# Performance work log

Measured on AMD Instinct MI355X. Metric: run time of the kernel, lower is better.

## Reference

```python
import jax, jax.numpy as jnp
from jax import lax
import numpy as np

B, L_IN, L_OUT, N, COV = 16, 96, 24, 320, 4
E, H = 64, 128
CIN = E + COV


def setup_inputs() -> dict:
    key = jax.random.key(0)
    ks = jax.random.split(key, 16)
    s = 0.05
    inp = {
        'history_data': jax.random.normal(ks[0], (B, L_IN, N, 1 + COV), jnp.float32),
        'future_data': jax.random.normal(ks[1], (B, L_OUT, N, 1 + COV), jnp.float32),
        'We': jax.random.normal(ks[2], (E, 1), jnp.float32) * s,
        'be': jnp.zeros((E,), jnp.float32),
        'Wih0': jax.random.normal(ks[3], (4 * H, CIN), jnp.float32) * s,
        'Whh0': jax.random.normal(ks[4], (4 * H, H), jnp.float32) * s,
        'bih0': jnp.zeros((4 * H,), jnp.float32),
        'bhh0': jnp.zeros((4 * H,), jnp.float32),
        'Wih1': jax.random.normal(ks[5], (4 * H, H), jnp.float32) * s,
        'Whh1': jax.random.normal(ks[6], (4 * H, H), jnp.float32) * s,
        'bih1': jnp.zeros((4 * H,), jnp.float32),
        'bhh1': jnp.zeros((4 * H,), jnp.float32),
        'Wh': jax.random.normal(ks[7], (2, H), jnp.float32) * s,
        'bh': jnp.zeros((2,), jnp.float32),
        'train': 1,
    }
    return inp


def _run_layer(xs, Wih, Whh, bih, bhh):
    # xs: [T, BN, Cin] -> ys: [T, BN, H]
    h0 = jnp.zeros((xs.shape[1], Whh.shape[1]), xs.dtype)

    def step(carry, x):
        h, c = carry
        g = x @ Wih.T + bih + h @ Whh.T + bhh  # [BN, 4H]
        i, f, gg, o = jnp.split(g, 4, axis=-1)  # torch gate order i,f,g,o
        c = jax.nn.sigmoid(f) * c + jax.nn.sigmoid(i) * jnp.tanh(gg)
        h = jax.nn.sigmoid(o) * jnp.tanh(c)
        return (h, c), h

    (_, _), ys = lax.scan(step, (h0, h0), xs)
    return ys


def reference(history_data, future_data, We, be, Wih0, Whh0, bih0, bhh0,
              Wih1, Whh1, bih1, bhh1, Wh, bh, train):
    # train branch (teacher forcing): history_next is always ground truth
    T = L_IN + L_OUT
    tgt = jnp.concatenate([history_data[..., 0:1], future_data[..., 0:1]], axis=1)  # [B,T,N,1]
    cov = jnp.concatenate([history_data[..., 1:], future_data[..., 1:]], axis=1)   # [B,T,N,COV]
    # step t uses target at t-1 and covariates at t, for t = 1..T-1
    embed = tgt[:, :T - 1] @ We.T + be                       # [B,T-1,N,E]
    enc_in = jnp.concatenate([embed, cov[:, 1:T]], axis=-1)  # [B,T-1,N,CIN]
    xs = enc_in.transpose(1, 0, 2, 3).reshape(T - 1, B * N, CIN)
    ys = _run_layer(xs, Wih0, Whh0, bih0, bhh0)
    ys = _run_layer(ys, Wih1, Whh1, bih1, bhh1)
    hid = jax.nn.relu(ys)                                    # [T-1, BN, H]
    head = hid @ Wh.T + bh                                   # [T-1, BN, 2]
    mu = head[..., 0:1]
    sigma = jax.nn.softplus(head[..., 1:2])
    p = jnp.concatenate([mu, sigma], axis=-1)
    p = p[-L_OUT:].reshape(L_OUT, B, N, 2).transpose(1, 0, 2, 3)  # [B,L_out,N,2]
    return p
```

## Files before the change

### kernel.cpp

```cpp
#include <hip/hip_runtime.h>

typedef __bf16 bf16x8 __attribute__((ext_vector_type(8)));
typedef unsigned short us8 __attribute__((ext_vector_type(8)));
typedef float f32x4 __attribute__((ext_vector_type(4)));

#define NROW 32
#define A_STR 136
#define NSTEP 119

__device__ __forceinline__ unsigned short f2bf(float f){
  unsigned int x = __builtin_bit_cast(unsigned int, f);
  x += 0x7fffu + ((x >> 16) & 1u);
  return (unsigned short)(x >> 16);
}
__device__ __forceinline__ float bf2f(unsigned short s){
  unsigned int x = ((unsigned int)s) << 16;
  return __builtin_bit_cast(float, x);
}
__device__ __forceinline__ float sigm(float x){ return 1.0f/(1.0f + __expf(-x)); }
__device__ __forceinline__ float tanh_(float x){ float e = __expf(2.0f*x); return 1.0f - 2.0f/(e + 1.0f); }

__device__ __forceinline__ f32x4 MFMA(us8 a, us8 b, f32x4 c){
  return __builtin_amdgcn_mfma_f32_16x16x32_bf16(
      __builtin_bit_cast(bf16x8, a), __builtin_bit_cast(bf16x8, b), c, 0, 0, 0);
}

struct SharedMem {
  unsigned short A0[2][NROW*A_STR];
  unsigned short A1[2][NROW*A_STR];
  unsigned short Ax[2][NROW][32];
  unsigned short xw[512*8];
  float c_lds[2][2][512][4];
  float b1[512];
  float Wh2f[256];
  float red[NROW][16][2];
  float we_s[64];
  float be_s[64];
  float bh_s[2];
};

__global__ __launch_bounds__(512)
__attribute__((amdgpu_waves_per_eu(2, 2)))
void deepar_kernel(
    const float* __restrict__ hist, const float* __restrict__ fut,
    const float* __restrict__ We,   const float* __restrict__ be,
    const float* __restrict__ Wih0, const float* __restrict__ Whh0,
    const float* __restrict__ bih0, const float* __restrict__ bhh0,
    const float* __restrict__ Wih1, const float* __restrict__ Whh1,
    const float* __restrict__ bih1, const float* __restrict__ bhh1,
    const float* __restrict__ Wh,   const float* __restrict__ bh,
    float* __restrict__ out)
{
  __shared__ SharedMem S;
  const int tid = threadIdx.x;
  const int wg  = blockIdx.x;
  const int b   = wg / 10;
  const int n0  = (wg % 10) * NROW;
  const int w   = tid >> 6;
  const int l   = tid & 63;
  const int gq  = l >> 4;
  const int r   = l & 15;

  {
    us8 z = {0,0,0,0,0,0,0,0};
    us8* pA0 = (us8*)&S.A0[0][0];
    us8* pA1 = (us8*)&S.A1[0][0];
    for (int i = tid; i < 2*NROW*A_STR/8; i += 512){ pA0[i] = z; pA1[i] = z; }
    us8* pAx = (us8*)&S.Ax[0][0][0];
    for (int i = tid; i < 2*NROW*32/8; i += 512) pAx[i] = z;
    f32x4 zf = {0.f,0.f,0.f,0.f};
    #pragma unroll
    for (int q = 0; q < 4; ++q) *(f32x4*)&S.c_lds[q >> 1][q & 1][tid][0] = zf;
  }
  if (tid < 64)       S.we_s[tid]       = We[tid];
  else if (tid < 128) S.be_s[tid - 64]  = be[tid - 64];
  else if (tid < 384) S.Wh2f[tid - 128] = Wh[tid - 128];
  else if (tid < 386) S.bh_s[tid - 384] = bh[tid - 384];
  __syncthreads();

  {
    const float* wr = Wih0 + tid * 68;
    float u = 0.f, v = 0.f;
    #pragma unroll 8
    for (int e = 0; e < 64; ++e){
      float wv = wr[e];
      u = fmaf(wv, S.we_s[e], u);
      v = fmaf(wv, S.be_s[e], v);
    }
    v += bih0[tid] + bhh0[tid];
    unsigned short* xp = &S.xw[tid * 8];
    xp[0] = f2bf(u);
    xp[1] = f2bf(wr[64]); xp[2] = f2bf(wr[65]); xp[3] = f2bf(wr[66]); xp[4] = f2bf(wr[67]);
    xp[5] = f2bf(v);
    xp[6] = 0; xp[7] = 0;
    S.b1[tid] = bih1[tid] + bhh1[tid];
  }
  if (tid < 64){ int row = tid >> 1, bsel = tid & 1; S.Ax[bsel][row][5] = 0x3F80; }
  if (tid < 160){
    int srow, sch, tau;
    if (tid < 32){ srow = tid; sch = 0; tau = 0; }
    else { int k = tid - 32; srow = k >> 2; sch = 1 + (k & 3); tau = 1; }
    const float* p = hist + ((b*96 + tau)*320 + n0 + srow)*5;
    S.Ax[0][srow][sch] = f2bf(p[sch]);
  }

  us8 WB[3][4][4];
  #pragma unroll
  for (int m = 0; m < 3; ++m){
    const float* base = (m == 0) ? Whh0 : (m == 1) ? Wih1 : Whh1;
    #pragma unroll
    for (int g = 0; g < 4; ++g){
      int col = g*128 + w*16 + r;
      #pragma unroll
      for (int q = 0; q < 4; ++q){
        const float* p = base + col*128 + q*32 + gq*8;
        f32x4 x0 = *(const f32x4*)p;
        f32x4 x1 = *(const f32x4*)(p + 4);
        us8 tt;
        tt[0]=f2bf(x0[0]); tt[1]=f2bf(x0[1]); tt[2]=f2bf(x0[2]); tt[3]=f2bf(x0[3]);
        tt[4]=f2bf(x1[0]); tt[5]=f2bf(x1[1]); tt[6]=f2bf(x1[2]); tt[7]=f2bf(x1[3]);
        WB[m][g][q] = tt;
      }
    }
  }

  __syncthreads();

  for (int t = 0; t < NSTEP; ++t){
    const int pb = t & 1, nb = pb ^ 1;
    const unsigned short* A0r = S.A0[pb];
    unsigned short*       A0w = S.A0[nb];
    const unsigned short* A1r = S.A1[pb];
    unsigned short*       A1w = S.A1[nb];

    float stv = 0.f; int sto = -1;
    if (t + 1 < NSTEP && tid < 160){
      int srow, sch, tau;
      if (tid < 32){ srow = tid; sch = 0; tau = t + 1; }
      else { int k = tid - 32; srow = k >> 2; sch = 1 + (k & 3); tau = t + 2; }
      const float* p = (tau < 96) ? (hist + ((b*96 + tau)*320 + n0 + srow)*5)
                                  : (fut  + ((b*24 + (tau - 96))*320 + n0 + srow)*5);
      stv = p[sch];
      sto = nb*NROW*32 + srow*32 + sch;
    }

    #pragma unroll
    for (int rt = 0; rt < 2; ++rt){
      const int rbase = rt * 16;
      f32x4 cprev = *(const f32x4*)&S.c_lds[0][rt][tid][0];
      f32x4 acc[4];
      us8 ax = *(const us8*)&S.Ax[pb][rbase + r][gq*8];
      #pragma unroll
      for (int g = 0; g < 4; ++g){
        us8 bx = *(const us8*)&S.xw[(g*128 + w*16 + r)*8];
        f32x4 z = {0.f,0.f,0.f,0.f};
        acc[g] = MFMA(ax, bx, z);
      }
      #pragma unroll
      for (int q = 0; q < 4; ++q){
        us8 a = *(const us8*)&A0r[(rbase + r)*A_STR + q*32 + gq*8];
        #pragma unroll
        for (int g = 0; g < 4; ++g) acc[g] = MFMA(a, WB[0][g][q], acc[g]);
      }
      f32x4 cnew;
      #pragma unroll
      for (int j = 0; j < 4; ++j){
        float c = fmaf(sigm(acc[1][j]), cprev[j], sigm(acc[0][j]) * tanh_(acc[2][j]));
        cnew[j] = c;
        float h = sigm(acc[3][j]) * tanh_(c);
        A0w[(rbase + gq*4 + j)*A_STR + w*16 + r] = f2bf(h);
      }
      *(f32x4*)&S.c_lds[0][rt][tid][0] = cnew;
    }
    __syncthreads();

    #pragma unroll
    for (int rt = 0; rt < 2; ++rt){
      const int rbase = rt * 16;
      f32x4 cprev = *(const f32x4*)&S.c_lds[1][rt][tid][0];
      float b1v = S.b1[w*16 + r];
      f32x4 acc[4];
      #pragma unroll
      for (int g = 0; g < 4; ++g){
        float bv = S.b1[g*128 + w*16 + r];
        f32x4 iv = {bv, bv, bv, bv};
        acc[g] = iv;
      }
      (void)b1v;
      #pragma unroll
      for (int q = 0; q < 4; ++q){
        us8 a = *(const us8*)&A0w[(rbase + r)*A_STR + q*32 + gq*8];
        #pragma unroll
        for (int g = 0; g < 4; ++g) acc[g] = MFMA(a, WB[1][g][q], acc[g]);
      }
      #pragma unroll
      for (int q = 0; q < 4; ++q){
        us8 a = *(const us8*)&A1r[(rbase + r)*A_STR + q*32 + gq*8];
        #pragma unroll
        for (int g = 0; g < 4; ++g) acc[g] = MFMA(a, WB[2][g][q], acc[g]);
      }
      f32x4 cnew;
      #pragma unroll
      for (int j = 0; j < 4; ++j){
        float c = fmaf(sigm(acc[1][j]), cprev[j], sigm(acc[0][j]) * tanh_(acc[2][j]));
        cnew[j] = c;
        float h = sigm(acc[3][j]) * tanh_(c);
        A1w[(rbase + gq*4 + j)*A_STR + w*16 + r] = f2bf(h);
      }
      *(f32x4*)&S.c_lds[1][rt][tid][0] = cnew;
    }
    if (sto >= 0) ((unsigned short*)&S.Ax[0][0][0])[sto] = f2bf(stv);
    __syncthreads();

    if (t >= 95){
      const int rown = tid >> 4, cg = tid & 15;
      us8 hv = *(const us8*)&A1w[rown*A_STR + cg*8];
      f32x4 wA0 = *(const f32x4*)&S.Wh2f[cg*8];
      f32x4 wA1 = *(const f32x4*)&S.Wh2f[cg*8 + 4];
      f32x4 wB0 = *(const f32x4*)&S.Wh2f[128 + cg*8];
      f32x4 wB1 = *(const f32x4*)&S.Wh2f[128 + cg*8 + 4];
      float pm = 0.f, ps = 0.f;
      #pragma unroll
      for (int k = 0; k < 4; ++k){
        float h0v = bf2f(hv[k]);     h0v = h0v > 0.f ? h0v : 0.f;
        float h1v = bf2f(hv[4 + k]); h1v = h1v > 0.f ? h1v : 0.f;
        pm = fmaf(h0v, wA0[k], pm);  pm = fmaf(h1v, wA1[k], pm);
        ps = fmaf(h0v, wB0[k], ps);  ps = fmaf(h1v, wB1[k], ps);
      }
      S.red[rown][cg][0] = pm; S.red[rown][cg][1] = ps;
      __syncthreads();
      if (tid < 64){
        int row = tid >> 1, o = tid & 1;
        float s = S.bh_s[o];
        #pragma unroll
        for (int k = 0; k < 16; ++k) s += S.red[row][k][o];
        if (o) s = (s > 15.f) ? s : __logf(1.0f + __expf(s));
        out[((b*24 + (t - 95))*320 + (n0 + row))*2 + o] = s;
      }
    }
  }
}

extern "C" void kernel_launch(void* const* d_in, const int* in_sizes, int n_in,
                              void* d_out, int out_size, void* d_ws, size_t ws_size,
                              hipStream_t stream) {
  const float* hist = (const float*)d_in[0];
  const float* fut  = (const float*)d_in[1];
  const float* We   = (const float*)d_in[2];
  const float* be   = (const float*)d_in[3];
  const float* Wih0 = (const float*)d_in[4];
  const float* Whh0 = (const float*)d_in[5];
  const float* bih0 = (const float*)d_in[6];
  const float* bhh0 = (const float*)d_in[7];
  const float* Wih1 = (const float*)d_in[8];
  const float* Whh1 = (const float*)d_in[9];
  const float* bih1 = (const float*)d_in[10];
  const float* bhh1 = (const float*)d_in[11];
  const float* Wh   = (const float*)d_in[12];
  const float* bh   = (const float*)d_in[13];
  float* out = (float*)d_out;

  deepar_kernel<<<dim3(160), dim3(512), 0, stream>>>(
      hist, fut, We, be, Wih0, Whh0, bih0, bhh0,
      Wih1, Whh1, bih1, bhh1, Wh, bh, out);
}
```

Baseline: 972.4 us.

## Move half of Whh0 weights to LDS and feed layer-1 weights from AGPRs

Half of the layer-0 recurrent weight fragments now live in a padded LDS table instead of registers, and the layer-1 MFMAs use inline asm that takes the B operand from AGPRs, with manual s_nop hazard padding. This relieves VGPR pressure so the 48 persistent weight fragments no longer spill or constrain scheduling. The Ax row stride is padded, and the layer-1 bias is hoisted out of the loop. In exchange, each step adds LDS reads for the weights, and the hand-placed nops and operand constraints can be fragile.

```diff
diff --git a/kernel.cpp b/kernel.cpp
--- a/kernel.cpp
+++ b/kernel.cpp
@@ -6,6 +6,8 @@
 
 #define NROW 32
 #define A_STR 136
+#define AX_STR 40
+#define WL_STR 521
 #define NSTEP 119
 
 __device__ __forceinline__ unsigned short f2bf(float f){
@@ -24,12 +26,23 @@
   return __builtin_amdgcn_mfma_f32_16x16x32_bf16(
       __builtin_bit_cast(bf16x8, a), __builtin_bit_cast(bf16x8, b), c, 0, 0, 0);
 }
+__device__ __forceinline__ void mfma_ag_first(f32x4& d, us8 a, us8 b){
+  asm("s_nop 1\n\tv_mfma_f32_16x16x32_bf16 %0, %1, %2, %0" : "+v"(d) : "v"(a), "a"(b));
+}
+__device__ __forceinline__ void mfma_ag(f32x4& d, us8 a, us8 b){
+  asm("v_mfma_f32_16x16x32_bf16 %0, %1, %2, %0" : "+v"(d) : "v"(a), "a"(b));
+}
+__device__ __forceinline__ void accfence4(f32x4& a0, f32x4& a1, f32x4& a2, f32x4& a3){
+  asm("s_nop 7\n\ts_nop 7\n\ts_nop 2"
+      : "+v"(a0), "+v"(a1), "+v"(a2), "+v"(a3));
+}
 
 struct SharedMem {
   unsigned short A0[2][NROW*A_STR];
   unsigned short A1[2][NROW*A_STR];
-  unsigned short Ax[2][NROW][32];
+  unsigned short Ax[2][NROW][AX_STR];
   unsigned short xw[512*8];
+  unsigned short W0l[8*WL_STR*8];
   float c_lds[2][2][512][4];
   float b1[512];
   float Wh2f[256];
@@ -60,6 +73,7 @@
   const int l   = tid & 63;
   const int gq  = l >> 4;
   const int r   = l & 15;
+  const int cw  = w * 16;
 
   {
     us8 z = {0,0,0,0,0,0,0,0};
@@ -67,7 +81,7 @@
     us8* pA1 = (us8*)&S.A1[0][0];
     for (int i = tid; i < 2*NROW*A_STR/8; i += 512){ pA0[i] = z; pA1[i] = z; }
     us8* pAx = (us8*)&S.Ax[0][0][0];
-    for (int i = tid; i < 2*NROW*32/8; i += 512) pAx[i] = z;
+    for (int i = tid; i < 2*NROW*AX_STR/8; i += 512) pAx[i] = z;
     f32x4 zf = {0.f,0.f,0.f,0.f};
     #pragma unroll
     for (int q = 0; q < 4; ++q) *(f32x4*)&S.c_lds[q >> 1][q & 1][tid][0] = zf;
@@ -95,6 +109,16 @@
     xp[6] = 0; xp[7] = 0;
     S.b1[tid] = bih1[tid] + bhh1[tid];
   }
+  for (int idx = tid; idx < 8*512; idx += 512){
+    int qgq = idx >> 9, col = idx & 511;
+    const float* p = Whh0 + col*128 + qgq*8;
+    f32x4 x0 = *(const f32x4*)p;
+    f32x4 x1 = *(const f32x4*)(p + 4);
+    us8 tt;
+    tt[0]=f2bf(x0[0]); tt[1]=f2bf(x0[1]); tt[2]=f2bf(x0[2]); tt[3]=f2bf(x0[3]);
+    tt[4]=f2bf(x1[0]); tt[5]=f2bf(x1[1]); tt[6]=f2bf(x1[2]); tt[7]=f2bf(x1[3]);
+    *(us8*)&S.W0l[(qgq*WL_STR + col)*8] = tt;
+  }
   if (tid < 64){ int row = tid >> 1, bsel = tid & 1; S.Ax[bsel][row][5] = 0x3F80; }
   if (tid < 160){
     int srow, sch, tau;
@@ -104,27 +128,34 @@
     S.Ax[0][srow][sch] = f2bf(p[sch]);
   }
 
-  us8 WB[3][4][4];
+  us8 WV[4][2], WA1[4][4], WA2[4][4];
   #pragma unroll
   for (int m = 0; m < 3; ++m){
     const float* base = (m == 0) ? Whh0 : (m == 1) ? Wih1 : Whh1;
     #pragma unroll
     for (int g = 0; g < 4; ++g){
-      int col = g*128 + w*16 + r;
+      int col = g*128 + cw + r;
       #pragma unroll
       for (int q = 0; q < 4; ++q){
+        if (m == 0 && q < 2) continue;
         const float* p = base + col*128 + q*32 + gq*8;
         f32x4 x0 = *(const f32x4*)p;
         f32x4 x1 = *(const f32x4*)(p + 4);
         us8 tt;
         tt[0]=f2bf(x0[0]); tt[1]=f2bf(x0[1]); tt[2]=f2bf(x0[2]); tt[3]=f2bf(x0[3]);
         tt[4]=f2bf(x1[0]); tt[5]=f2bf(x1[1]); tt[6]=f2bf(x1[2]); tt[7]=f2bf(x1[3]);
-        WB[m][g][q] = tt;
+        if (m == 0)      WV[g][q-2] = tt;
+        else if (m == 1) WA1[g][q]  = tt;
+        else             WA2[g][q]  = tt;
       }
     }
   }
 
   __syncthreads();
+
+  float b1g[4];
+  #pragma unroll
+  for (int g = 0; g < 4; ++g) b1g[g] = S.b1[g*128 + cw + r];
 
   for (int t = 0; t < NSTEP; ++t){
     const int pb = t & 1, nb = pb ^ 1;
@@ -141,34 +172,44 @@
       const float* p = (tau < 96) ? (hist + ((b*96 + tau)*320 + n0 + srow)*5)
                                   : (fut  + ((b*24 + (tau - 96))*320 + n0 + srow)*5);
       stv = p[sch];
-      sto = nb*NROW*32 + srow*32 + sch;
+      sto = nb*NROW*AX_STR + srow*AX_STR + sch;
     }
 
     #pragma unroll
     for (int rt = 0; rt < 2; ++rt){
       const int rbase = rt * 16;
-      f32x4 cprev = *(const f32x4*)&S.c_lds[0][rt][tid][0];
       f32x4 acc[4];
       us8 ax = *(const us8*)&S.Ax[pb][rbase + r][gq*8];
       #pragma unroll
       for (int g = 0; g < 4; ++g){
-        us8 bx = *(const us8*)&S.xw[(g*128 + w*16 + r)*8];
+        us8 bx = *(const us8*)&S.xw[(g*128 + cw + r)*8];
         f32x4 z = {0.f,0.f,0.f,0.f};
         acc[g] = MFMA(ax, bx, z);
       }
       #pragma unroll
-      for (int q = 0; q < 4; ++q){
+      for (int q = 0; q < 2; ++q){
         us8 a = *(const us8*)&A0r[(rbase + r)*A_STR + q*32 + gq*8];
         #pragma unroll
-        for (int g = 0; g < 4; ++g) acc[g] = MFMA(a, WB[0][g][q], acc[g]);
-      }
+        for (int g = 0; g < 4; ++g){
+          us8 bw = *(const us8*)&S.W0l[((q*4 + gq)*WL_STR + g*128 + cw + r)*8];
+          acc[g] = MFMA(a, bw, acc[g]);
+        }
+      }
+      #pragma unroll
+      for (int q = 2; q < 4; ++q){
+        us8 a = *(const us8*)&A0r[(rbase + r)*A_STR + q*32 + gq*8];
+        #pragma unroll
+        for (int g = 0; g < 4; ++g)
+          acc[g] = MFMA(a, WV[g][q-2], acc[g]);
+      }
+      f32x4 cprev = *(const f32x4*)&S.c_lds[0][rt][tid][0];
       f32x4 cnew;
       #pragma unroll
       for (int j = 0; j < 4; ++j){
         float c = fmaf(sigm(acc[1][j]), cprev[j], sigm(acc[0][j]) * tanh_(acc[2][j]));
         cnew[j] = c;
         float h = sigm(acc[3][j]) * tanh_(c);
-        A0w[(rbase + gq*4 + j)*A_STR + w*16 + r] = f2bf(h);
+        A0w[(rbase + gq*4 + j)*A_STR + cw + r] = f2bf(h);
       }
       *(f32x4*)&S.c_lds[0][rt][tid][0] = cnew;
     }
@@ -177,35 +218,40 @@
     #pragma unroll
     for (int rt = 0; rt < 2; ++rt){
       const int rbase = rt * 16;
-      f32x4 cprev = *(const f32x4*)&S.c_lds[1][rt][tid][0];
-      float b1v = S.b1[w*16 + r];
       f32x4 acc[4];
       #pragma unroll
       for (int g = 0; g < 4; ++g){
-        float bv = S.b1[g*128 + w*16 + r];
-        f32x4 iv = {bv, bv, bv, bv};
+        f32x4 iv = {b1g[g], b1g[g], b1g[g], b1g[g]};
         acc[g] = iv;
       }
-      (void)b1v;
-      #pragma unroll
-      for (int q = 0; q < 4; ++q){
+      {
+        us8 a = *(const us8*)&A0w[(rbase + r)*A_STR + 0*32 + gq*8];
+        mfma_ag_first(acc[0], a, WA1[0][0]);
+        mfma_ag(acc[1], a, WA1[1][0]);
+        mfma_ag(acc[2], a, WA1[2][0]);
+        mfma_ag(acc[3], a, WA1[3][0]);
+      }
+      #pragma unroll
+      for (int q = 1; q < 4; ++q){
         us8 a = *(const us8*)&A0w[(rbase + r)*A_STR + q*32 + gq*8];
         #pragma unroll
-        for (int g = 0; g < 4; ++g) acc[g] = MFMA(a, WB[1][g][q], acc[g]);
+        for (int g = 0; g < 4; ++g) mfma_ag(acc[g], a, WA1[g][q]);
       }
       #pragma unroll
       for (int q = 0; q < 4; ++q){
         us8 a = *(const us8*)&A1r[(rbase + r)*A_STR + q*32 + gq*8];
         #pragma unroll
-        for (int g = 0; g < 4; ++g) acc[g] = MFMA(a, WB[2][g][q], acc[g]);
-      }
+        for (int g = 0; g < 4; ++g) mfma_ag(acc[g], a, WA2[g][q]);
+      }
+      accfence4(acc[0], acc[1], acc[2], acc[3]);
+      f32x4 cprev = *(const f32x4*)&S.c_lds[1][rt][tid][0];
       f32x4 cnew;
       #pragma unroll
       for (int j = 0; j < 4; ++j){
         float c = fmaf(sigm(acc[1][j]), cprev[j], sigm(acc[0][j]) * tanh_(acc[2][j]));
         cnew[j] = c;
         float h = sigm(acc[3][j]) * tanh_(c);
-        A1w[(rbase + gq*4 + j)*A_STR + w*16 + r] = f2bf(h);
+        A1w[(rbase + gq*4 + j)*A_STR + cw + r] = f2bf(h);
       }
       *(f32x4*)&S.c_lds[1][rt][tid][0] = cnew;
     }
@@ -216,7 +262,7 @@
       const int rown = tid >> 4, cg = tid & 15;
       us8 hv = *(const us8*)&A1w[rown*A_STR + cg*8];
       f32x4 wA0 = *(const f32x4*)&S.Wh2f[cg*8];
-      f32x4 wA1 = *(const f32x4*)&S.Wh2f[cg*8 + 4];
+      f32x4 wA1v = *(const f32x4*)&S.Wh2f[cg*8 + 4];
       f32x4 wB0 = *(const f32x4*)&S.Wh2f[128 + cg*8];
       f32x4 wB1 = *(const f32x4*)&S.Wh2f[128 + cg*8 + 4];
       float pm = 0.f, ps = 0.f;
@@ -224,7 +270,7 @@
       for (int k = 0; k < 4; ++k){
         float h0v = bf2f(hv[k]);     h0v = h0v > 0.f ? h0v : 0.f;
         float h1v = bf2f(hv[4 + k]); h1v = h1v > 0.f ? h1v : 0.f;
-        pm = fmaf(h0v, wA0[k], pm);  pm = fmaf(h1v, wA1[k], pm);
+        pm = fmaf(h0v, wA0[k], pm);  pm = fmaf(h1v, wA1v[k], pm);
         ps = fmaf(h0v, wB0[k], ps);  ps = fmaf(h1v, wB1[k], ps);
       }
       S.red[rown][cg][0] = pm; S.red[rown][cg][1] = ps;
```

Result: slower. 1.107 ms (+13.8%).
